# Optimization experiments

Measured on AMD Instinct MI355X. Metric: run time of the kernel, lower is better.

Reference implementation:

```python
import jax, jax.numpy as jnp
import numpy as np
from jax import lax

N, CIN, COUT, H, W = 16, 512, 256, 32, 32
EPS = 1e-5


def _conv(x, w, b, pad_h, pad_w):
    # x: [N,Cin,H,W], w: [Cout,Cin,kh,kw], pad = ((top,bottom),(left,right))
    y = lax.conv_general_dilated(
        x, w, window_strides=(1, 1), padding=(pad_h, pad_w),
        dimension_numbers=("NCHW", "OIHW", "NCHW"))
    return y + b[None, :, None, None]


def setup_inputs() -> dict:
    key = jax.random.key(0)
    ks = jax.random.split(key, 12)
    s = 0.02
    return {
        "x": jax.random.normal(ks[0], (N, CIN, H, W), jnp.float32),
        "w1": jax.random.normal(ks[1], (COUT, CIN, 3, 3), jnp.float32) * s,
        "b1": jax.random.normal(ks[2], (COUT,), jnp.float32) * s,
        "w2": jax.random.normal(ks[3], (COUT, CIN, 2, 3), jnp.float32) * s,
        "b2": jax.random.normal(ks[4], (COUT,), jnp.float32) * s,
        "w3": jax.random.normal(ks[5], (COUT, CIN, 3, 2), jnp.float32) * s,
        "b3": jax.random.normal(ks[6], (COUT,), jnp.float32) * s,
        "w4": jax.random.normal(ks[7], (COUT, CIN, 2, 2), jnp.float32) * s,
        "b4": jax.random.normal(ks[8], (COUT,), jnp.float32) * s,
        "gamma": jnp.ones((COUT,), jnp.float32),
        "beta": jnp.zeros((COUT,), jnp.float32),
    }


def reference(x, w1, b1, w2, b2, w3, b3, w4, b4, gamma, beta):
    # torch F.pad(l,r,t,b) -> lax padding ((top,bottom),(left,right))
    o1 = _conv(x, w1, b1, (1, 1), (1, 1))  # 3x3, pad (1,1,1,1) -> [N,Cout,H,W]
    o2 = _conv(x, w2, b2, (1, 0), (1, 1))  # 2x3, pad (1,1,1,0)
    o3 = _conv(x, w3, b3, (1, 1), (1, 0))  # 3x2, pad (1,0,1,1)
    o4 = _conv(x, w4, b4, (1, 0), (1, 0))  # 2x2, pad (1,0,1,0)
    # pixel-shuffle interleave: o1->(even,even), o2->(odd,even), o3->(even,odd), o4->(odd,odd)
    row_even = jnp.stack([o1, o3], axis=-1).reshape(N, COUT, H, 2 * W)
    row_odd = jnp.stack([o2, o4], axis=-1).reshape(N, COUT, H, 2 * W)
    y = jnp.stack([row_even, row_odd], axis=-2).reshape(N, COUT, 2 * H, 2 * W)
    # BatchNorm2d, training mode: biased batch stats over (N,H,W)
    mean = jnp.mean(y, axis=(0, 2, 3), keepdims=True)
    var = jnp.mean(jnp.square(y - mean), axis=(0, 2, 3), keepdims=True)
    normed = (y - mean) * lax.rsqrt(var + EPS)
    normed = normed * gamma[None, :, None, None] + beta[None, :, None, None]
    return jax.nn.relu(normed)
```

## Files before the change

kernel.cpp:

```cpp
#include <hip/hip_runtime.h>
#include <hip/hip_bf16.h>


typedef unsigned short ushort_t;
typedef __attribute__((ext_vector_type(8))) short short8;
typedef __attribute__((ext_vector_type(4))) float floatx4;
typedef __attribute__((ext_vector_type(2))) float floatx2;
typedef __attribute__((ext_vector_type(4))) unsigned short u16x4;
typedef __attribute__((ext_vector_type(8))) unsigned short u16x8;
typedef __attribute__((ext_vector_type(4))) unsigned int u32x4;

#define XT_OFF    0u
#define WT_OFF    18939904u
#define BIAS_OFF  28377088u
#define STATS_OFF 28381184u

#define NSITES_P0 204
#define NSITES_P1 170

#define ASYNC16(g, l) __builtin_amdgcn_global_load_lds( \
    (const __attribute__((address_space(1))) void*)(g), \
    (__attribute__((address_space(3))) void*)(l), 16, 0, 0)

#define ISSUE_FENCE asm volatile("" ::: "memory")

#define WAITBAR4 \
  asm volatile("s_waitcnt vmcnt(4) lgkmcnt(0)\n\ts_barrier" ::: "memory")
#define WAITBAR0 \
  asm volatile("s_waitcnt vmcnt(0) lgkmcnt(0)\n\ts_barrier" ::: "memory")

__device__ __forceinline__ ushort_t f2bf(float f) {
  unsigned int u = __builtin_bit_cast(unsigned int, f);
  u += 0x7fffu + ((u >> 16) & 1u);
  return (ushort_t)(u >> 16);
}

__global__ __launch_bounds__(256) void prep_all(
    const float* __restrict__ x, ushort_t* __restrict__ xt,
    const float* __restrict__ w1, const float* __restrict__ w2,
    const float* __restrict__ w3, const float* __restrict__ w4,
    const float* __restrict__ b1, const float* __restrict__ b2,
    const float* __restrict__ b3, const float* __restrict__ b4,
    ushort_t* __restrict__ wt, float* __restrict__ bias,
    float* __restrict__ stats) {
  __shared__ ushort_t lds[128 * 36];
  const int blk = blockIdx.x;
  const int t = threadIdx.x;
  if (blk < 1024) {
    const int q = blk >> 8, co = blk & 255;
    const int row = ((q & 1) << 9) + (co << 1) + (q >> 1);
    if (blk == 0) { stats[t] = 0.f; stats[t + 256] = 0.f; }
    const float* wsrc; const float* bsrc; int khl, kwl;
    if (q == 0)      { wsrc = w1; bsrc = b1; khl = 3; kwl = 3; }
    else if (q == 1) { wsrc = w2; bsrc = b2; khl = 2; kwl = 3; }
    else if (q == 2) { wsrc = w3; bsrc = b3; khl = 3; kwl = 2; }
    else             { wsrc = w4; bsrc = b4; khl = 2; kwl = 2; }
    if (t == 0) bias[row] = bsrc[co];
    ushort_t* dst = wt + (size_t)row * 4608;
    for (int tap = 0; tap < 9; ++tap) {
      const int dh = tap / 3, dw = tap % 3;
      const bool valid = (dh < khl) && (dw < kwl);
#pragma unroll
      for (int cc = 0; cc < 2; ++cc) {
        const int ci = cc * 256 + t;
        ushort_t v = 0;
        if (valid)
          v = f2bf(wsrc[(((size_t)co * 512 + ci) * khl + dh) * kwl + dw]);
        dst[tap * 512 + ci] = v;
      }
    }
    return;
  }
  const int b = blk - 1024;
  const int n = b / 34, hp = b % 34;
  ushort_t* dst = xt + (size_t)(n * 34 + hp) * (34 * 512);
  if (hp == 0 || hp == 33) {
    u32x4 z = {0u, 0u, 0u, 0u};
    for (int i = t; i < 2176; i += 256) ((u32x4*)dst)[i] = z;
    return;
  }
  const int h = hp - 1;
  {
    u32x4 z = {0u, 0u, 0u, 0u};
    if (t < 64) ((u32x4*)dst)[t] = z;
    else if (t < 128) ((u32x4*)(dst + 33 * 512))[t - 64] = z;
  }
  const size_t base = (size_t)n * 524288 + (size_t)h * 32;
  for (int ci0 = 0; ci0 < 512; ci0 += 128) {
    __syncthreads();
    {
      const int cil = t >> 3;
      const int w4 = (t & 7) << 2;
#pragma unroll
      for (int cc = 0; cc < 4; ++cc) {
        const int ci = cil + cc * 32;
        floatx4 v = *(const floatx4*)(x + base + (size_t)(ci0 + ci) * 1024 + w4);
        u16x4 hv;
#pragma unroll
        for (int j = 0; j < 4; ++j) hv[j] = f2bf(v[j]);
        *(u16x4*)&lds[ci * 36 + w4] = hv;
      }
    }
    __syncthreads();
    {
      const int w = t & 31;
      const int j8 = t >> 5;
#pragma unroll
      for (int cc2 = 0; cc2 < 2; ++cc2) {
        const int cil = cc2 * 64 + j8 * 8;
        u16x8 v;
#pragma unroll
        for (int j = 0; j < 8; ++j) v[j] = lds[(cil + j) * 36 + w];
        *(u16x8*)(dst + (w + 1) * 512 + ci0 + cil) = v;
      }
    }
  }
}

template <int NTAPS, int NSITES_T>
__device__ __forceinline__ void gemm_body(
    const ushort_t* __restrict__ xt, const ushort_t* __restrict__ wt,
    const float* __restrict__ bias, float* __restrict__ out,
    float* __restrict__ stats, char* ldsX, char* ldsW,
    int bn, int bm) {
  const int tid = threadIdx.x;
  const int n0 = bn << 7;
  const int n_img = bm >> 3;
  const int h0p = (bm & 7) << 2;
  const int wv = tid >> 6, lane = tid & 63;
  const int ri = lane & 15, kg = lane >> 4;
  const int wm = (wv & 1) << 6, wn = (wv >> 1) << 6;

  constexpr int XTOT = NSITES_T * 8;
  constexpr int XFP = XTOT / 256;
  constexpr int XTL = XTOT - XFP * 256;

  const char* xgp[XFP + 1];
  char* xlp[XFP + 1];
  {
    const char* xg = (const char*)(xt + (size_t)(n_img * 34 + h0p) * (34 * 512));
#pragma unroll
    for (int p = 0; p < XFP + 1; ++p) {
      const int idx = p * 256 + tid;
      const int site = idx >> 3, slot = idx & 7;
      const int c = slot ^ (site & 7);
      xgp[p] = xg + site * 1024 + (c << 4);
      xlp[p] = ldsX + idx * 16;
    }
  }
  const char* wgp[4];
#pragma unroll
  for (int p = 0; p < 4; ++p) {
    const int idx = p * 256 + tid;
    const int row = idx >> 3, slot = idx & 7;
    const int c = slot ^ (row & 7);
    wgp[p] = (const char*)wt + (size_t)(n0 + row) * 9216 + (c << 4);
  }
  char* const wl = ldsW + tid * 16;

  floatx4 acc[4][4] = {};

  int arow[4], bsite[4];
#pragma unroll
  for (int f = 0; f < 4; ++f) arow[f] = wn + (f << 4) + ri;
#pragma unroll
  for (int fj = 0; fj < 4; ++fj)
    bsite[fj] = ((wm >> 5) + (fj >> 1)) * 34 + ((fj & 1) << 4) + ri;

  for (int chunk = 0; chunk < 8; ++chunk) {
    const int cb = chunk << 7;
#pragma unroll
    for (int p = 0; p < XFP; ++p) ASYNC16(xgp[p] + cb, xlp[p]);
    if (tid < XTL) ASYNC16(xgp[XFP] + cb, xlp[XFP]);
    ISSUE_FENCE;
#pragma unroll
    for (int p = 0; p < 4; ++p) ASYNC16(wgp[p] + cb, wl + p * 4096);
    ISSUE_FENCE;
#pragma unroll
    for (int p = 0; p < 4; ++p)
      ASYNC16(wgp[p] + cb + 1024, wl + 16384 + p * 4096);
    WAITBAR4;
#pragma unroll
    for (int tap = 0; tap < NTAPS; ++tap) {
      if (tap + 2 < NTAPS) {
        const int noff = ((tap + 2) << 10) + cb;
        char* const wld = ldsW + ((tap + 2) % 3) * 16384 + tid * 16;
#pragma unroll
        for (int p = 0; p < 4; ++p) ASYNC16(wgp[p] + noff, wld + p * 4096);
      }
      const char* wb = ldsW + (tap % 3) * 16384;
      const int tsite = (tap / 3) * 34 + (tap % 3);
#pragma unroll
      for (int ks = 0; ks < 2; ++ks) {
        const int c = (ks << 2) + kg;
        short8 a4[4], b4[4];
#pragma unroll
        for (int f = 0; f < 4; ++f)
          a4[f] = *(const short8*)(wb + arow[f] * 128 +
                                   ((c ^ (arow[f] & 7)) << 4));
#pragma unroll
        for (int fj = 0; fj < 4; ++fj) {
          const int srow = bsite[fj] + tsite;
          b4[fj] = *(const short8*)(ldsX + srow * 128 + ((c ^ (srow & 7)) << 4));
        }
#pragma unroll
        for (int fi = 0; fi < 4; ++fi)
#pragma unroll
          for (int fj = 0; fj < 4; ++fj)
            acc[fi][fj] = __builtin_amdgcn_mfma_f32_16x16x32_bf16(
                a4[fi], b4[fj], acc[fi][fj], 0, 0, 0);
      }
      if (tap + 2 < NTAPS) { WAITBAR4; } else { WAITBAR0; }
    }
  }

  const int quad = kg, colL = ri;
  const int dh6 = (bn >> 2) << 6;
#pragma unroll
  for (int fi = 0; fi < 4; ++fi) {
    const int rbase = n0 + wn + (fi << 4) + (quad << 2);
    const floatx4 bv = *(const floatx4*)(bias + rbase);
    const int co = (rbase & 511) >> 1;
    float sA = 0.f, s2A = 0.f, sB = 0.f, s2B = 0.f;
    float* ob = out + (((size_t)(n_img * 256 + co)) << 12) + dh6;
#pragma unroll
    for (int fj = 0; fj < 4; ++fj) {
      const int mb = wm + (fj << 4) + colL;
      const int h = h0p + (mb >> 5), w = mb & 31;
      const float v0 = acc[fi][fj][0] + bv[0];
      const float v1 = acc[fi][fj][1] + bv[1];
      const float v2 = acc[fi][fj][2] + bv[2];
      const float v3 = acc[fi][fj][3] + bv[3];
      sA += v0 + v1;
      s2A += v0 * v0 + v1 * v1;
      sB += v2 + v3;
      s2B += v2 * v2 + v3 * v3;
      float* p = ob + (h << 7) + (w << 1);
      floatx2 eA = {v0, v1};
      floatx2 eB = {v2, v3};
      *(floatx2*)p = eA;
      *(floatx2*)(p + 4096) = eB;
    }
#pragma unroll
    for (int off = 1; off < 16; off <<= 1) {
      sA += __shfl_xor(sA, off);
      s2A += __shfl_xor(s2A, off);
      sB += __shfl_xor(sB, off);
      s2B += __shfl_xor(s2B, off);
    }
    if (colL == 0) {
      atomicAdd(&stats[co], sA);
      atomicAdd(&stats[256 + co], s2A);
      atomicAdd(&stats[co + 1], sB);
      atomicAdd(&stats[256 + co + 1], s2B);
    }
  }
}

__global__ __launch_bounds__(256) void gemm_kernel(
    const ushort_t* __restrict__ xt, const ushort_t* __restrict__ wt,
    const float* __restrict__ bias, float* __restrict__ out,
    float* __restrict__ stats) {
  __shared__ char ldsX[NSITES_P0 * 128];
  __shared__ char ldsW[3][128 * 128];
  const int bx = blockIdx.x;
  const int bn = (bx & 7) ^ (((bx >> 9) & 1) << 2);
  const int bm = (bx >> 3) & 127;
  if (bn < 4)
    gemm_body<9, NSITES_P0>(xt, wt, bias, out, stats,
                            ldsX, ldsW[0], bn, bm);
  else
    gemm_body<6, NSITES_P1>(xt, wt, bias, out, stats,
                            ldsX, ldsW[0], bn, bm);
}

__global__ __launch_bounds__(256) void bn_apply(
    float* __restrict__ y, const float* __restrict__ stats,
    const float* __restrict__ gamma, const float* __restrict__ beta) {
  const int b = blockIdx.x;
  const int co = b & 255;
  const int t = threadIdx.x;
  const float mean = stats[co] * (1.f / 65536.f);
  const float var = stats[256 + co] * (1.f / 65536.f) - mean * mean;
  const float rstd = rsqrtf(var + 1e-5f);
  const float scale = rstd * gamma[co];
  const float shift = beta[co] - mean * scale;
  float* p = y + (size_t)b * 4096;
#pragma unroll
  for (int it = 0; it < 4; ++it) {
    floatx4* q = (floatx4*)(p + (it * 256 + t) * 4);
    floatx4 v = *q;
#pragma unroll
    for (int e = 0; e < 4; ++e) v[e] = fmaxf(v[e] * scale + shift, 0.f);
    *q = v;
  }
}

extern "C" void kernel_launch(void* const* d_in, const int* in_sizes, int n_in,
                              void* d_out, int out_size, void* d_ws,
                              size_t ws_size, hipStream_t stream) {
  const float* x  = (const float*)d_in[0];
  const float* w1 = (const float*)d_in[1];
  const float* b1 = (const float*)d_in[2];
  const float* w2 = (const float*)d_in[3];
  const float* b2 = (const float*)d_in[4];
  const float* w3 = (const float*)d_in[5];
  const float* b3 = (const float*)d_in[6];
  const float* w4 = (const float*)d_in[7];
  const float* b4 = (const float*)d_in[8];
  const float* gamma = (const float*)d_in[9];
  const float* beta  = (const float*)d_in[10];
  float* out = (float*)d_out;

  char* ws = (char*)d_ws;
  ushort_t* xt   = (ushort_t*)(ws + XT_OFF);
  ushort_t* wt   = (ushort_t*)(ws + WT_OFF);
  float*    bias = (float*)(ws + BIAS_OFF);
  float*    st   = (float*)(ws + STATS_OFF);

  prep_all<<<1568, 256, 0, stream>>>(x, xt, w1, w2, w3, w4,
                                     b1, b2, b3, b4, wt, bias, st);
  gemm_kernel<<<1024, 256, 0, stream>>>(xt, wt, bias, out, st);
  bn_apply<<<4096, 256, 0, stream>>>(out, st, gamma, beta);
}
```

Baseline: 264.4 us.

## Merge both output-parity panels into one block sharing the input tile

Each GEMM block now computes both row-parity panels (9-tap and 6-tap) for the same 128 output channels using two accumulator sets. One staged input-site tile in LDS serves 15 weight-tap segments instead of being loaded by two separate blocks, and the grid is halved. This removes the duplicated input loading and the imbalance between the 9-tap and 6-tap block types. In exchange it doubles accumulator register pressure (which may hurt occupancy) and assumes the weight layout places the second panel at a fixed WPAN offset.

```diff
diff --git a/kernel.cpp b/kernel.cpp
--- a/kernel.cpp
+++ b/kernel.cpp
@@ -15,8 +15,8 @@
 #define BIAS_OFF  28377088u
 #define STATS_OFF 28381184u
 
-#define NSITES_P0 204
-#define NSITES_P1 170
+#define NSITES 204
+#define WPAN   4718592u
 
 #define ASYNC16(g, l) __builtin_amdgcn_global_load_lds( \
     (const __attribute__((address_space(1))) void*)(g), \
@@ -117,30 +117,54 @@
   }
 }
 
-template <int NTAPS, int NSITES_T>
-__device__ __forceinline__ void gemm_body(
+__device__ __forceinline__ void mfma_seg(
+    const char* wb, const char* ldsX, const int (&arow)[4],
+    const int (&bsite)[4], int tsite, int kg, floatx4 (&acc)[4][4]) {
+#pragma unroll
+  for (int ks = 0; ks < 2; ++ks) {
+    const int c = (ks << 2) + kg;
+    short8 a4[4], b4[4];
+#pragma unroll
+    for (int f = 0; f < 4; ++f)
+      a4[f] = *(const short8*)(wb + arow[f] * 128 +
+                               ((c ^ (arow[f] & 7)) << 4));
+#pragma unroll
+    for (int fj = 0; fj < 4; ++fj) {
+      const int srow = bsite[fj] + tsite;
+      b4[fj] = *(const short8*)(ldsX + srow * 128 + ((c ^ (srow & 7)) << 4));
+    }
+#pragma unroll
+    for (int fi = 0; fi < 4; ++fi)
+#pragma unroll
+      for (int fj = 0; fj < 4; ++fj)
+        acc[fi][fj] = __builtin_amdgcn_mfma_f32_16x16x32_bf16(
+            a4[fi], b4[fj], acc[fi][fj], 0, 0, 0);
+  }
+}
+
+__global__ __launch_bounds__(256) void gemm_kernel(
     const ushort_t* __restrict__ xt, const ushort_t* __restrict__ wt,
     const float* __restrict__ bias, float* __restrict__ out,
-    float* __restrict__ stats, char* ldsX, char* ldsW,
-    int bn, int bm) {
+    float* __restrict__ stats) {
+  __shared__ char ldsX[NSITES * 128];
+  __shared__ char ldsW[3][128 * 128];
   const int tid = threadIdx.x;
-  const int n0 = bn << 7;
+  const int bx = blockIdx.x;
+  const int bn2 = bx & 3;
+  const int bm = bx >> 2;
+  const int n0 = bn2 << 7;
   const int n_img = bm >> 3;
   const int h0p = (bm & 7) << 2;
   const int wv = tid >> 6, lane = tid & 63;
   const int ri = lane & 15, kg = lane >> 4;
   const int wm = (wv & 1) << 6, wn = (wv >> 1) << 6;
 
-  constexpr int XTOT = NSITES_T * 8;
-  constexpr int XFP = XTOT / 256;
-  constexpr int XTL = XTOT - XFP * 256;
-
-  const char* xgp[XFP + 1];
-  char* xlp[XFP + 1];
+  const char* xgp[7];
+  char* xlp[7];
   {
     const char* xg = (const char*)(xt + (size_t)(n_img * 34 + h0p) * (34 * 512));
 #pragma unroll
-    for (int p = 0; p < XFP + 1; ++p) {
+    for (int p = 0; p < 7; ++p) {
       const int idx = p * 256 + tid;
       const int site = idx >> 3, slot = idx & 7;
       const int c = slot ^ (site & 7);
@@ -156,9 +180,10 @@
     const int c = slot ^ (row & 7);
     wgp[p] = (const char*)wt + (size_t)(n0 + row) * 9216 + (c << 4);
   }
-  char* const wl = ldsW + tid * 16;
-
-  floatx4 acc[4][4] = {};
+  char* const wl = ldsW[0] + tid * 16;
+
+  floatx4 accA[4][4] = {};
+  floatx4 accB[4][4] = {};
 
   int arow[4], bsite[4];
 #pragma unroll
@@ -167,111 +192,91 @@
   for (int fj = 0; fj < 4; ++fj)
     bsite[fj] = ((wm >> 5) + (fj >> 1)) * 34 + ((fj & 1) << 4) + ri;
 
+  constexpr int NT = 15;
+  constexpr int tapof[NT] = {0, 0, 1, 1, 2, 2, 3, 3, 4, 4, 5, 5, 6, 7, 8};
+  constexpr int pof[NT]   = {0, 1, 0, 1, 0, 1, 0, 1, 0, 1, 0, 1, 0, 0, 0};
+
   for (int chunk = 0; chunk < 8; ++chunk) {
     const int cb = chunk << 7;
 #pragma unroll
-    for (int p = 0; p < XFP; ++p) ASYNC16(xgp[p] + cb, xlp[p]);
-    if (tid < XTL) ASYNC16(xgp[XFP] + cb, xlp[XFP]);
+    for (int p = 0; p < 6; ++p) ASYNC16(xgp[p] + cb, xlp[p]);
+    if (tid < 96) ASYNC16(xgp[6] + cb, xlp[6]);
     ISSUE_FENCE;
 #pragma unroll
     for (int p = 0; p < 4; ++p) ASYNC16(wgp[p] + cb, wl + p * 4096);
     ISSUE_FENCE;
 #pragma unroll
     for (int p = 0; p < 4; ++p)
-      ASYNC16(wgp[p] + cb + 1024, wl + 16384 + p * 4096);
+      ASYNC16(wgp[p] + WPAN + cb, wl + 16384 + p * 4096);
     WAITBAR4;
 #pragma unroll
-    for (int tap = 0; tap < NTAPS; ++tap) {
-      if (tap + 2 < NTAPS) {
-        const int noff = ((tap + 2) << 10) + cb;
-        char* const wld = ldsW + ((tap + 2) % 3) * 16384 + tid * 16;
+    for (int i = 0; i < NT; ++i) {
+      if (i + 2 < NT) {
+        const size_t noff =
+            (size_t)(pof[i + 2] ? WPAN : 0u) + (tapof[i + 2] << 10) + cb;
+        char* const wld = ldsW[0] + ((i + 2) % 3) * 16384 + tid * 16;
 #pragma unroll
         for (int p = 0; p < 4; ++p) ASYNC16(wgp[p] + noff, wld + p * 4096);
       }
-      const char* wb = ldsW + (tap % 3) * 16384;
-      const int tsite = (tap / 3) * 34 + (tap % 3);
-#pragma unroll
-      for (int ks = 0; ks < 2; ++ks) {
-        const int c = (ks << 2) + kg;
-        short8 a4[4], b4[4];
-#pragma unroll
-        for (int f = 0; f < 4; ++f)
-          a4[f] = *(const short8*)(wb + arow[f] * 128 +
-                                   ((c ^ (arow[f] & 7)) << 4));
-#pragma unroll
-        for (int fj = 0; fj < 4; ++fj) {
-          const int srow = bsite[fj] + tsite;
-          b4[fj] = *(const short8*)(ldsX + srow * 128 + ((c ^ (srow & 7)) << 4));
-        }
-#pragma unroll
-        for (int fi = 0; fi < 4; ++fi)
-#pragma unroll
-          for (int fj = 0; fj < 4; ++fj)
-            acc[fi][fj] = __builtin_amdgcn_mfma_f32_16x16x32_bf16(
-                a4[fi], b4[fj], acc[fi][fj], 0, 0, 0);
-      }
-      if (tap + 2 < NTAPS) { WAITBAR4; } else { WAITBAR0; }
+      const char* wb = ldsW[0] + (i % 3) * 16384;
+      const int tsite = (tapof[i] / 3) * 34 + (tapof[i] % 3);
+      if (pof[i] == 0)
+        mfma_seg(wb, ldsX, arow, bsite, tsite, kg, accA);
+      else
+        mfma_seg(wb, ldsX, arow, bsite, tsite, kg, accB);
+      if (i + 2 < NT) { WAITBAR4; } else { WAITBAR0; }
     }
   }
 
   const int quad = kg, colL = ri;
-  const int dh6 = (bn >> 2) << 6;
 #pragma unroll
   for (int fi = 0; fi < 4; ++fi) {
     const int rbase = n0 + wn + (fi << 4) + (quad << 2);
-    const floatx4 bv = *(const floatx4*)(bias + rbase);
-    const int co = (rbase & 511) >> 1;
-    float sA = 0.f, s2A = 0.f, sB = 0.f, s2B = 0.f;
-    float* ob = out + (((size_t)(n_img * 256 + co)) << 12) + dh6;
+    const floatx4 bvA = *(const floatx4*)(bias + rbase);
+    const floatx4 bvB = *(const floatx4*)(bias + 512 + rbase);
+    const int co = rbase >> 1;
+    float s0 = 0.f, q0 = 0.f, s1 = 0.f, q1 = 0.f;
+    float* ob = out + (((size_t)(n_img * 256 + co)) << 12);
 #pragma unroll
     for (int fj = 0; fj < 4; ++fj) {
       const int mb = wm + (fj << 4) + colL;
       const int h = h0p + (mb >> 5), w = mb & 31;
-      const float v0 = acc[fi][fj][0] + bv[0];
-      const float v1 = acc[fi][fj][1] + bv[1];
-      const float v2 = acc[fi][fj][2] + bv[2];
-      const float v3 = acc[fi][fj][3] + bv[3];
-      sA += v0 + v1;
-      s2A += v0 * v0 + v1 * v1;
-      sB += v2 + v3;
-      s2B += v2 * v2 + v3 * v3;
+      const float vA0 = accA[fi][fj][0] + bvA[0];
+      const float vA1 = accA[fi][fj][1] + bvA[1];
+      const float vA2 = accA[fi][fj][2] + bvA[2];
+      const float vA3 = accA[fi][fj][3] + bvA[3];
+      const float vB0 = accB[fi][fj][0] + bvB[0];
+      const float vB1 = accB[fi][fj][1] + bvB[1];
+      const float vB2 = accB[fi][fj][2] + bvB[2];
+      const float vB3 = accB[fi][fj][3] + bvB[3];
+      s0 += (vA0 + vA1) + (vB0 + vB1);
+      q0 += vA0 * vA0 + vA1 * vA1 + vB0 * vB0 + vB1 * vB1;
+      s1 += (vA2 + vA3) + (vB2 + vB3);
+      q1 += vA2 * vA2 + vA3 * vA3 + vB2 * vB2 + vB3 * vB3;
       float* p = ob + (h << 7) + (w << 1);
-      floatx2 eA = {v0, v1};
-      floatx2 eB = {v2, v3};
-      *(floatx2*)p = eA;
-      *(floatx2*)(p + 4096) = eB;
+      floatx2 eA0 = {vA0, vA1};
+      floatx2 eB0 = {vB0, vB1};
+      floatx2 eA1 = {vA2, vA3};
+      floatx2 eB1 = {vB2, vB3};
+      *(floatx2*)p = eA0;
+      *(floatx2*)(p + 64) = eB0;
+      *(floatx2*)(p + 4096) = eA1;
+      *(floatx2*)(p + 4160) = eB1;
     }
 #pragma unroll
     for (int off = 1; off < 16; off <<= 1) {
-      sA += __shfl_xor(sA, off);
-      s2A += __shfl_xor(s2A, off);
-      sB += __shfl_xor(sB, off);
-      s2B += __shfl_xor(s2B, off);
+      s0 += __shfl_xor(s0, off);
+      q0 += __shfl_xor(q0, off);
+      s1 += __shfl_xor(s1, off);
+      q1 += __shfl_xor(q1, off);
     }
     if (colL == 0) {
-      atomicAdd(&stats[co], sA);
-      atomicAdd(&stats[256 + co], s2A);
-      atomicAdd(&stats[co + 1], sB);
-      atomicAdd(&stats[256 + co + 1], s2B);
-    }
-  }
-}
-
-__global__ __launch_bounds__(256) void gemm_kernel(
-    const ushort_t* __restrict__ xt, const ushort_t* __restrict__ wt,
-    const float* __restrict__ bias, float* __restrict__ out,
-    float* __restrict__ stats) {
-  __shared__ char ldsX[NSITES_P0 * 128];
-  __shared__ char ldsW[3][128 * 128];
-  const int bx = blockIdx.x;
-  const int bn = (bx & 7) ^ (((bx >> 9) & 1) << 2);
-  const int bm = (bx >> 3) & 127;
-  if (bn < 4)
-    gemm_body<9, NSITES_P0>(xt, wt, bias, out, stats,
-                            ldsX, ldsW[0], bn, bm);
-  else
-    gemm_body<6, NSITES_P1>(xt, wt, bias, out, stats,
-                            ldsX, ldsW[0], bn, bm);
+      atomicAdd(&stats[co], s0);
+      atomicAdd(&stats[256 + co], q0);
+      atomicAdd(&stats[co + 1], s1);
+      atomicAdd(&stats[256 + co + 1], q1);
+    }
+  }
 }
 
 __global__ __launch_bounds__(256) void bn_apply(
@@ -320,6 +325,6 @@
 
   prep_all<<<1568, 256, 0, stream>>>(x, xt, w1, w2, w3, w4,
                                      b1, b2, b3, b4, wt, bias, st);
-  gemm_kernel<<<1024, 256, 0, stream>>>(xt, wt, bias, out, st);
+  gemm_kernel<<<512, 256, 0, stream>>>(xt, wt, bias, out, st);
   bn_apply<<<4096, 256, 0, stream>>>(out, st, gamma, beta);
 }
```

Result: slower. 320.6 us (+21.2%).
